# Kernel optimization log

Hardware: AMD Instinct MI355X
Metric: run time of the kernel (lower is better)

## Reference

```python
import jax, jax.numpy as jnp
import numpy as np

NUM_CLASSES = 10000
EMBED_DIM = 128
BATCH = 4096
SCALE = 10.0
FOCAL_ALPHA = 0.25
FOCAL_GAMMA = 2.0
HARD_NEG_RATIO = 0.3


def setup_inputs() -> dict:
    key = jax.random.key(0)
    k1, k2, k3, k4 = jax.random.split(key, 4)
    embeddings = jax.random.normal(k1, (BATCH, EMBED_DIM), dtype=jnp.float32)
    labels = jax.random.randint(k2, (BATCH,), 0, NUM_CLASSES)
    class_weights = jax.random.uniform(k3, (NUM_CLASSES,), dtype=jnp.float32)
    # kaiming_normal_(mode='fan_out') on [C, D] -> std = sqrt(2 / C)
    proxies = jax.random.normal(k4, (NUM_CLASSES, EMBED_DIM), dtype=jnp.float32) * np.sqrt(2.0 / NUM_CLASSES)
    return {"embeddings": embeddings, "labels": labels,
            "class_weights": class_weights, "proxies": proxies}


def reference(embeddings, labels, class_weights, proxies):
    C = proxies.shape[0]
    # L2 normalize (F.normalize with eps=1e-12)
    e = embeddings / jnp.maximum(jnp.linalg.norm(embeddings, axis=1, keepdims=True), 1e-12)
    p = proxies / jnp.maximum(jnp.linalg.norm(proxies, axis=1, keepdims=True), 1e-12)
    sim = jnp.einsum('bd,cd->bc', e, p) * SCALE  # [B, C]

    pos_sim = jnp.take_along_axis(sim, labels[:, None], axis=1)[:, 0]  # [B]

    # mask out the positive class, then top-k hard negatives (k is static)
    k = max(1, int((C - 1) * HARD_NEG_RATIO))
    is_pos = labels[:, None] == jnp.arange(C)[None, :]
    neg_sim = jnp.where(is_pos, -jnp.inf, sim)
    hard_neg, _ = jax.lax.top_k(neg_sim, k)  # [B, k]

    combined = jnp.concatenate([pos_sim[:, None], hard_neg], axis=1)  # [B, 1+k]
    probs = jax.nn.softmax(combined, axis=1)
    pos_prob = probs[:, 0]

    ce = -jnp.log(pos_prob + 1e-8)
    focal = FOCAL_ALPHA * (1.0 - pos_prob) ** FOCAL_GAMMA * ce
    weighted = focal * class_weights[labels]
    return jnp.sum(weighted) / embeddings.shape[0]
```

## Files before the change

### kernel.cpp

```cpp
#include <hip/hip_runtime.h>
#include <hip/hip_bf16.h>
#include <hip/hip_fp16.h>


#define BATCH   4096
#define NCLASS  10000
#define EDIM    128
#define KSEL    2999
#define LDK     136
#define MLOG    10.0f

typedef __attribute__((ext_vector_type(8))) short short8;
typedef __attribute__((ext_vector_type(4))) float floatx4;

__device__ __forceinline__ unsigned short f2bf(float f) {
    unsigned int u = __float_as_uint(f);
    unsigned int r = (u + 0x7FFFu + ((u >> 16) & 1u)) >> 16;
    return (unsigned short)r;
}
__device__ __forceinline__ unsigned int f2key16(float x) {
    unsigned short hb = __half_as_ushort(__float2half(x));
    return (hb & 0x8000u) ? (unsigned int)(~hb & 0xFFFFu)
                          : (unsigned int)(hb | 0x8000u);
}
__device__ __forceinline__ float key16val(unsigned int k) {
    unsigned short hb = (k & 0x8000u) ? (unsigned short)(k ^ 0x8000u)
                                      : (unsigned short)(~k & 0xFFFFu);
    return __half2float(__ushort_as_half(hb));
}

__global__ __launch_bounds__(256) void prep_kernel(
    const float* __restrict__ emb, const float* __restrict__ px,
    unsigned short* __restrict__ px_bf, unsigned short* __restrict__ emb_bf)
{
    const int tid  = threadIdx.x;
    const int lane = tid & 63;
    const int w    = tid >> 6;
    const int row  = blockIdx.x * 4 + w;

    const float* src;
    unsigned short* dst;
    float scale;
    if (row < NCLASS) {
        src = px + (size_t)row * EDIM;  dst = px_bf + (size_t)row * EDIM;  scale = 1.0f;
    } else {
        int r = row - NCLASS;
        src = emb + (size_t)r * EDIM;   dst = emb_bf + (size_t)r * EDIM;   scale = 10.0f;
    }
    float2 v = *(const float2*)(src + 2 * lane);
    float ss = v.x * v.x + v.y * v.y;
    #pragma unroll
    for (int off = 32; off; off >>= 1) ss += __shfl_xor(ss, off);
    float inv = scale / fmaxf(sqrtf(ss), 1e-12f);
    ushort2 o;
    o.x = f2bf(v.x * inv);
    o.y = f2bf(v.y * inv);
    *(ushort2*)(dst + 2 * lane) = o;
}

__global__ __launch_bounds__(256, 3) void gemm_kernel(
    const unsigned short* __restrict__ emb_bf,
    const unsigned short* __restrict__ px_bf,
    unsigned short* __restrict__ simk, int row0, int nby)
{
    __shared__ __align__(16) unsigned short T[128 * LDK];

    const int NBX = (NCLASS + 127) / 128;
    const int tid  = threadIdx.x;
    const int lane = tid & 63;
    const int w    = tid >> 6;

    int ct, rt;
    {
        int L = blockIdx.x;
        if ((nby & 7) == 0) {
            int rpx = nby >> 3;
            int xcd = L & 7;
            int s   = L >> 3;
            rt = xcd * rpx + (s % rpx);
            ct = s / rpx;
        } else {
            ct = L % NBX; rt = L / NBX;
        }
    }
    const int c0   = ct * 128;
    const int rg0  = row0 + rt * 128;

    const int wr = (w >> 1) * 64;
    const int wc = (w & 1) * 64;
    const int fm = lane & 15;
    const int fq = lane >> 4;

    const unsigned short* arow[4];
    const unsigned short* brow[4];
    #pragma unroll
    for (int i = 0; i < 4; ++i)
        arow[i] = emb_bf + (size_t)(rg0 + wr + i * 16 + fm) * EDIM + fq * 8;
    #pragma unroll
    for (int j = 0; j < 4; ++j) {
        int col = c0 + wc + j * 16 + fm;
        if (col > NCLASS - 1) col = NCLASS - 1;
        brow[j] = px_bf + (size_t)col * EDIM + fq * 8;
    }

    floatx4 acc[4][4];
    #pragma unroll
    for (int i = 0; i < 4; ++i)
        #pragma unroll
        for (int j = 0; j < 4; ++j)
            acc[i][j] = (floatx4){0.f, 0.f, 0.f, 0.f};

    short8 af[2][4], bf_[2][4];
    #pragma unroll
    for (int i = 0; i < 4; ++i) af[0][i]  = *(const short8*)(arow[i]);
    #pragma unroll
    for (int j = 0; j < 4; ++j) bf_[0][j] = *(const short8*)(brow[j]);

    #pragma unroll
    for (int kk = 0; kk < 4; ++kk) {
        const int cur = kk & 1, nxt = cur ^ 1;
        if (kk < 3) {
            const int kof = (kk + 1) * 32;
            #pragma unroll
            for (int i = 0; i < 4; ++i)
                af[nxt][i]  = *(const short8*)(arow[i] + kof);
            #pragma unroll
            for (int j = 0; j < 4; ++j)
                bf_[nxt][j] = *(const short8*)(brow[j] + kof);
        }
        #pragma unroll
        for (int i = 0; i < 4; ++i)
            #pragma unroll
            for (int j = 0; j < 4; ++j)
                acc[i][j] = __builtin_amdgcn_mfma_f32_16x16x32_bf16(
                    af[cur][i], bf_[cur][j], acc[i][j], 0, 0, 0);
    }

    #pragma unroll
    for (int j = 0; j < 4; ++j) {
        int col = wc + j * 16 + fm;
        #pragma unroll
        for (int i = 0; i < 4; ++i) {
            int rbase = wr + i * 16 + fq * 4;
            #pragma unroll
            for (int r = 0; r < 4; ++r)
                T[(rbase + r) * LDK + col] = (unsigned short)f2key16(acc[i][j][r]);
        }
    }
    __syncthreads();

    const int rl0 = rt * 128;
    #pragma unroll
    for (int t = 0; t < 8; ++t) {
        int idx = t * 256 + tid;
        int rowl = idx >> 4;
        int g    = idx & 15;
        int col  = c0 + g * 8;
        if (col < NCLASS) {
            uint4 v = *(const uint4*)(T + rowl * LDK + g * 8);
            *(uint4*)(simk + (size_t)(rl0 + rowl) * NCLASS + col) = v;
        }
    }
}

__global__ __launch_bounds__(256, 8) void select_kernel(
    const unsigned short* __restrict__ simk, const int* __restrict__ labels,
    const float* __restrict__ cw, float* __restrict__ partials, int row0)
{
    __shared__ __align__(16) unsigned int hist[2048];
    __shared__ __align__(16) unsigned int psum[256];
    __shared__ float fred[8];
    __shared__ float s_pos;
    __shared__ unsigned int s_b, s_fill, s_cntb;

    const int tid   = threadIdx.x;
    const int lane  = tid & 63;
    const int w     = tid >> 6;
    const int rl    = blockIdx.x;
    const int label = labels[row0 + rl];
    const unsigned short* srow = simk + (size_t)rl * NCLASS;

    unsigned short poskey = 0;
    if (tid == 0) poskey = srow[label];

    {
        uint4 z = make_uint4(0u, 0u, 0u, 0u);
        *(uint4*)&hist[tid * 8]     = z;
        *(uint4*)&hist[tid * 8 + 4] = z;
    }
    __syncthreads();
    uint4 kv[5];
    kv[4] = make_uint4(0u, 0u, 0u, 0u);
    #pragma unroll
    for (int t = 0; t < 5; ++t) {
        int i = tid + t * 256;
        if (i < NCLASS / 8) kv[t] = *(const uint4*)(srow + i * 8);
    }

    #pragma unroll
    for (int t = 0; t < 5; ++t) {
        int i = tid + t * 256;
        if (i < NCLASS / 8) {
            unsigned int p[4] = {kv[t].x, kv[t].y, kv[t].z, kv[t].w};
            #pragma unroll
            for (int q = 0; q < 4; ++q) {
                unsigned int klo = p[q] & 0xFFFFu;
                unsigned int khi = p[q] >> 16;
                atomicAdd(&hist[klo >> 5], 0x100000u | (klo & 31u));
                atomicAdd(&hist[khi >> 5], 0x100000u | (khi & 31u));
            }
        }
    }
    __syncthreads();
    if (tid == 0) {
        s_pos = key16val(poskey);
        hist[poskey >> 5] -= 0x100000u | ((unsigned int)poskey & 31u);
    }
    __syncthreads();

    uint4 h0 = *(const uint4*)&hist[tid * 8];
    uint4 h1 = *(const uint4*)&hist[tid * 8 + 4];
    unsigned int wd[8] = {h0.x, h0.y, h0.z, h0.w, h1.x, h1.y, h1.z, h1.w};
    unsigned int sfx[8];
    sfx[7] = wd[7] >> 20;
    #pragma unroll
    for (int i = 6; i >= 0; --i) sfx[i] = sfx[i + 1] + (wd[i] >> 20);
    psum[tid] = sfx[0];
    __syncthreads();
    if (w == 0) {
        uint4 g = *(const uint4*)&psum[lane * 4];
        unsigned int gs = g.x + g.y + g.z + g.w;
        unsigned int s = gs;
        #pragma unroll
        for (int off = 1; off < 64; off <<= 1) {
            unsigned int o = __shfl_down(s, off);
            if (lane + off < 64) s += o;
        }
        unsigned int above = s - gs;
        unsigned int a3 = above;
        unsigned int a2 = a3 + g.w;
        unsigned int a1 = a2 + g.z;
        unsigned int a0 = a1 + g.y;
        psum[lane * 4 + 0] = a0; psum[lane * 4 + 1] = a1;
        psum[lane * 4 + 2] = a2; psum[lane * 4 + 3] = a3;
    }
    __syncthreads();
    {
        unsigned int add = psum[tid];
        #pragma unroll
        for (int i = 0; i < 8; ++i) {
            unsigned int cur = sfx[i] + add;
            unsigned int nxt = ((i < 7) ? sfx[i + 1] : 0u) + add;
            if (cur >= KSEL && nxt < KSEL) {
                s_b    = (unsigned int)(tid * 8 + i);
                s_fill = KSEL - nxt;
                s_cntb = sfx[i] - ((i < 7) ? sfx[i + 1] : 0u);
            }
        }
    }
    __syncthreads();

    const unsigned int b = s_b;
    float sum = 0.f, bsum = 0.f;
    if (b >= 1024u) {
        const float fillf = (float)s_fill;
        #pragma unroll
        for (int i = 0; i < 8; ++i) {
            unsigned int bin = (unsigned int)(tid * 8 + i);
            unsigned int c = wd[i] >> 20;
            if (bin >= b && c) {
                float rbar = (float)(wd[i] & 0xFFFFFu) / (float)c;
                unsigned int kb = bin << 5;
                float v0  = key16val(kb);
                float v32 = key16val(kb + 32u);
                float vm  = v0 + (v32 - v0) * (rbar * 0.03125f);
                float e = __expf(vm - MLOG);
                sum += ((bin > b) ? (float)c : fillf) * e;
            }
        }
    } else {
        for (int i = tid; i < NCLASS / 8; i += 256) {
            uint4 pk = *(const uint4*)(srow + i * 8);
            unsigned int p[4] = {pk.x, pk.y, pk.z, pk.w};
            #pragma unroll
            for (int q = 0; q < 4; ++q) {
                unsigned int klo = p[q] & 0xFFFFu;
                unsigned int khi = p[q] >> 16;
                unsigned int blo = klo >> 5, bhi = khi >> 5;
                int idx = i * 8 + q * 2;
                if (blo >= b && idx != label) {
                    float e = __expf(key16val(klo) - MLOG);
                    if (blo > b) sum += e; else bsum += e;
                }
                if (bhi >= b && (idx + 1) != label) {
                    float e = __expf(key16val(khi) - MLOG);
                    if (bhi > b) sum += e; else bsum += e;
                }
            }
        }
    }
    #pragma unroll
    for (int off = 32; off; off >>= 1) {
        sum  += __shfl_xor(sum, off);
        bsum += __shfl_xor(bsum, off);
    }
    if (lane == 0) { fred[w] = sum; fred[4 + w] = bsum; }
    __syncthreads();

    if (tid == 0) {
        float S  = fred[0] + fred[1] + fred[2] + fred[3];
        float Bs = fred[4] + fred[5] + fred[6] + fred[7];
        float ep = __expf(s_pos - MLOG);
        float denom = S + Bs * ((float)s_fill / (float)s_cntb) + ep;
        float p  = ep / denom;
        float ce = -logf(p + 1e-8f);
        float focal = 0.25f * (1.0f - p) * (1.0f - p) * ce;
        partials[row0 + rl] = focal * cw[label] * (1.0f / (float)BATCH);
    }
}

__global__ __launch_bounds__(256) void reduce_kernel(
    const float* __restrict__ partials, float* __restrict__ out)
{
    __shared__ float red[4];
    const int tid = threadIdx.x;
    float s = 0.f;
    #pragma unroll
    for (int t = 0; t < BATCH / 256; ++t)
        s += partials[tid + t * 256];
    #pragma unroll
    for (int off = 32; off; off >>= 1) s += __shfl_xor(s, off);
    if ((tid & 63) == 0) red[tid >> 6] = s;
    __syncthreads();
    if (tid == 0) out[0] = red[0] + red[1] + red[2] + red[3];
}

extern "C" void kernel_launch(void* const* d_in, const int* in_sizes, int n_in,
                              void* d_out, int out_size, void* d_ws, size_t ws_size,
                              hipStream_t stream) {
    const float* emb    = (const float*)d_in[0];
    const int*   labels = (const int*)d_in[1];
    const float* cw     = (const float*)d_in[2];
    const float* px     = (const float*)d_in[3];
    float* out = (float*)d_out;
    char*  wsc = (char*)d_ws;

    unsigned short* px_bf  = (unsigned short*)wsc;
    unsigned short* emb_bf = (unsigned short*)(wsc + 2560000);
    float*          parts  = (float*)(wsc + 3608576);
    unsigned short* simk   = (unsigned short*)(wsc + 3624960);

    size_t fixed = 3624960;
    size_t avail = (ws_size > fixed) ? (ws_size - fixed) : 0;
    long long cap = (long long)(avail / ((size_t)NCLASS * 2));
    int chunk = (int)((cap / 128) * 128);
    if (chunk > BATCH) chunk = BATCH;
    if (chunk < 128) chunk = 128;

    prep_kernel<<<3524, 256, 0, stream>>>(emb, px, px_bf, emb_bf);

    const int NBX = (NCLASS + 127) / 128;
    for (int r0 = 0; r0 < BATCH; r0 += chunk) {
        int rows = (BATCH - r0 < chunk) ? (BATCH - r0) : chunk;
        int nby  = rows / 128;
        gemm_kernel<<<NBX * nby, 256, 0, stream>>>(emb_bf, px_bf, simk, r0, nby);
        select_kernel<<<rows, 256, 0, stream>>>(simk, labels, cw, parts, r0);
    }
    reduce_kernel<<<1, 256, 0, stream>>>(parts, out);
}
```

Baseline: 131.1 us.

## Stage proxy tile in LDS for GEMM and use nontemporal output stores

The GEMM kernel now loads the 128x128 bf16 proxy tile cooperatively into shared memory once. The MFMA loop reads B fragments from LDS instead of each wave fetching overlapping rows from global memory, and the same LDS buffer is reused for the output transpose after a barrier. It also raises the occupancy hint from 3 to 4 blocks per CU and writes the sim keys with nontemporal stores to reduce cache pollution. The cost is extra barriers and LDS traffic, and B is no longer prefetched ahead of use.

```diff
diff --git a/kernel.cpp b/kernel.cpp
--- a/kernel.cpp
+++ b/kernel.cpp
@@ -12,6 +12,7 @@
 
 typedef __attribute__((ext_vector_type(8))) short short8;
 typedef __attribute__((ext_vector_type(4))) float floatx4;
+typedef __attribute__((ext_vector_type(4))) unsigned int uintx4;
 
 __device__ __forceinline__ unsigned short f2bf(float f) {
     unsigned int u = __float_as_uint(f);
@@ -58,12 +59,12 @@
     *(ushort2*)(dst + 2 * lane) = o;
 }
 
-__global__ __launch_bounds__(256, 3) void gemm_kernel(
+__global__ __launch_bounds__(256, 4) void gemm_kernel(
     const unsigned short* __restrict__ emb_bf,
     const unsigned short* __restrict__ px_bf,
     unsigned short* __restrict__ simk, int row0, int nby)
 {
-    __shared__ __align__(16) unsigned short T[128 * LDK];
+    __shared__ __align__(16) unsigned short Bls[128 * LDK];
 
     const int NBX = (NCLASS + 127) / 128;
     const int tid  = threadIdx.x;
@@ -86,22 +87,32 @@
     const int c0   = ct * 128;
     const int rg0  = row0 + rt * 128;
 
+    #pragma unroll
+    for (int i = 0; i < 8; ++i) {
+        int c  = tid + i * 256;
+        int n  = c >> 4;
+        int kc = (c & 15) << 3;
+        uint4 v = make_uint4(0u, 0u, 0u, 0u);
+        if (c0 + n < NCLASS)
+            v = *(const uint4*)(px_bf + (size_t)(c0 + n) * EDIM + kc);
+        *(uint4*)(Bls + n * LDK + kc) = v;
+    }
+
     const int wr = (w >> 1) * 64;
     const int wc = (w & 1) * 64;
     const int fm = lane & 15;
     const int fq = lane >> 4;
 
     const unsigned short* arow[4];
-    const unsigned short* brow[4];
     #pragma unroll
     for (int i = 0; i < 4; ++i)
         arow[i] = emb_bf + (size_t)(rg0 + wr + i * 16 + fm) * EDIM + fq * 8;
-    #pragma unroll
-    for (int j = 0; j < 4; ++j) {
-        int col = c0 + wc + j * 16 + fm;
-        if (col > NCLASS - 1) col = NCLASS - 1;
-        brow[j] = px_bf + (size_t)col * EDIM + fq * 8;
-    }
+
+    short8 af[2][4];
+    #pragma unroll
+    for (int i = 0; i < 4; ++i) af[0][i] = *(const short8*)(arow[i]);
+
+    __syncthreads();
 
     floatx4 acc[4][4];
     #pragma unroll
@@ -109,33 +120,31 @@
         #pragma unroll
         for (int j = 0; j < 4; ++j)
             acc[i][j] = (floatx4){0.f, 0.f, 0.f, 0.f};
-
-    short8 af[2][4], bf_[2][4];
-    #pragma unroll
-    for (int i = 0; i < 4; ++i) af[0][i]  = *(const short8*)(arow[i]);
-    #pragma unroll
-    for (int j = 0; j < 4; ++j) bf_[0][j] = *(const short8*)(brow[j]);
 
     #pragma unroll
     for (int kk = 0; kk < 4; ++kk) {
         const int cur = kk & 1, nxt = cur ^ 1;
         if (kk < 3) {
-            const int kof = (kk + 1) * 32;
+            const int kof2 = (kk + 1) * 32;
             #pragma unroll
             for (int i = 0; i < 4; ++i)
-                af[nxt][i]  = *(const short8*)(arow[i] + kof);
-            #pragma unroll
-            for (int j = 0; j < 4; ++j)
-                bf_[nxt][j] = *(const short8*)(brow[j] + kof);
-        }
+                af[nxt][i] = *(const short8*)(arow[i] + kof2);
+        }
+        const int kof = kk * 32 + fq * 8;
+        short8 b[4];
+        #pragma unroll
+        for (int j = 0; j < 4; ++j)
+            b[j] = *(const short8*)(Bls + (wc + j * 16 + fm) * LDK + kof);
         #pragma unroll
         for (int i = 0; i < 4; ++i)
             #pragma unroll
             for (int j = 0; j < 4; ++j)
                 acc[i][j] = __builtin_amdgcn_mfma_f32_16x16x32_bf16(
-                    af[cur][i], bf_[cur][j], acc[i][j], 0, 0, 0);
-    }
-
+                    af[cur][i], b[j], acc[i][j], 0, 0, 0);
+    }
+
+    __syncthreads();
+    unsigned short* T = Bls;
     #pragma unroll
     for (int j = 0; j < 4; ++j) {
         int col = wc + j * 16 + fm;
@@ -157,8 +166,9 @@
         int g    = idx & 15;
         int col  = c0 + g * 8;
         if (col < NCLASS) {
-            uint4 v = *(const uint4*)(T + rowl * LDK + g * 8);
-            *(uint4*)(simk + (size_t)(rl0 + rowl) * NCLASS + col) = v;
+            uintx4 v = *(const uintx4*)(T + rowl * LDK + g * 8);
+            __builtin_nontemporal_store(v,
+                (uintx4*)(simk + (size_t)(rl0 + rowl) * NCLASS + col));
         }
     }
 }
```

New measurement: 139.5 us. 1.06x slower.

## Stage GEMM tiles into LDS via direct global-to-LDS loads with XOR swizzle

Applied to the files above, without the earlier changes.

The GEMM kernel now copies the full 128x128 A and B bf16 tiles into shared memory with global_load_lds (16-byte direct loads) using an XOR swizzle, then reads MFMA fragments from LDS instead of loading them from global memory into registers per wave. The goal is to remove duplicated global loads across waves and the register double-buffering, and to make the tile fetch coalesced. The output staging buffer now reuses the A tile region without padding, which may cause bank conflicts on the transpose writes. Shared memory grows to 64KB, and the occupancy hint of 3 blocks is dropped, which may lower occupancy.

```diff
diff --git a/kernel.cpp b/kernel.cpp
--- a/kernel.cpp
+++ b/kernel.cpp
@@ -7,7 +7,6 @@
 #define NCLASS  10000
 #define EDIM    128
 #define KSEL    2999
-#define LDK     136
 #define MLOG    10.0f
 
 typedef __attribute__((ext_vector_type(8))) short short8;
@@ -27,6 +26,13 @@
     unsigned short hb = (k & 0x8000u) ? (unsigned short)(k ^ 0x8000u)
                                       : (unsigned short)(~k & 0xFFFFu);
     return __half2float(__ushort_as_half(hb));
+}
+
+__device__ __forceinline__ void gload16(const unsigned short* g,
+                                        unsigned short* l) {
+    __builtin_amdgcn_global_load_lds(
+        (const __attribute__((address_space(1))) unsigned int*)g,
+        (__attribute__((address_space(3))) unsigned int*)l, 16, 0, 0);
 }
 
 __global__ __launch_bounds__(256) void prep_kernel(
@@ -58,12 +64,13 @@
     *(ushort2*)(dst + 2 * lane) = o;
 }
 
-__global__ __launch_bounds__(256, 3) void gemm_kernel(
+__global__ __launch_bounds__(256) void gemm_kernel(
     const unsigned short* __restrict__ emb_bf,
     const unsigned short* __restrict__ px_bf,
     unsigned short* __restrict__ simk, int row0, int nby)
 {
-    __shared__ __align__(16) unsigned short T[128 * LDK];
+    __shared__ __align__(16) unsigned short Als[128 * EDIM];
+    __shared__ __align__(16) unsigned short Bls[128 * EDIM];
 
     const int NBX = (NCLASS + 127) / 128;
     const int tid  = threadIdx.x;
@@ -86,23 +93,29 @@
     const int c0   = ct * 128;
     const int rg0  = row0 + rt * 128;
 
+    #pragma unroll
+    for (int i = 0; i < 8; ++i) {
+        int c   = tid + i * 256;
+        int r   = c >> 4;
+        int gsw = (c & 15) ^ (r & 7);
+        gload16(emb_bf + (size_t)(rg0 + r) * EDIM + gsw * 8, Als + c * 8);
+    }
+    #pragma unroll
+    for (int i = 0; i < 8; ++i) {
+        int c   = tid + i * 256;
+        int n   = c >> 4;
+        int gsw = (c & 15) ^ (n & 7);
+        int col = c0 + n;
+        if (col > NCLASS - 1) col = NCLASS - 1;
+        gload16(px_bf + (size_t)col * EDIM + gsw * 8, Bls + c * 8);
+    }
+    __syncthreads();
+
     const int wr = (w >> 1) * 64;
     const int wc = (w & 1) * 64;
     const int fm = lane & 15;
     const int fq = lane >> 4;
 
-    const unsigned short* arow[4];
-    const unsigned short* brow[4];
-    #pragma unroll
-    for (int i = 0; i < 4; ++i)
-        arow[i] = emb_bf + (size_t)(rg0 + wr + i * 16 + fm) * EDIM + fq * 8;
-    #pragma unroll
-    for (int j = 0; j < 4; ++j) {
-        int col = c0 + wc + j * 16 + fm;
-        if (col > NCLASS - 1) col = NCLASS - 1;
-        brow[j] = px_bf + (size_t)col * EDIM + fq * 8;
-    }
-
     floatx4 acc[4][4];
     #pragma unroll
     for (int i = 0; i < 4; ++i)
@@ -110,32 +123,26 @@
         for (int j = 0; j < 4; ++j)
             acc[i][j] = (floatx4){0.f, 0.f, 0.f, 0.f};
 
-    short8 af[2][4], bf_[2][4];
-    #pragma unroll
-    for (int i = 0; i < 4; ++i) af[0][i]  = *(const short8*)(arow[i]);
-    #pragma unroll
-    for (int j = 0; j < 4; ++j) bf_[0][j] = *(const short8*)(brow[j]);
-
     #pragma unroll
     for (int kk = 0; kk < 4; ++kk) {
-        const int cur = kk & 1, nxt = cur ^ 1;
-        if (kk < 3) {
-            const int kof = (kk + 1) * 32;
-            #pragma unroll
-            for (int i = 0; i < 4; ++i)
-                af[nxt][i]  = *(const short8*)(arow[i] + kof);
-            #pragma unroll
-            for (int j = 0; j < 4; ++j)
-                bf_[nxt][j] = *(const short8*)(brow[j] + kof);
-        }
+        const int go = ((kk * 4 + fq) ^ (fm & 7)) << 3;
+        short8 a[4], b[4];
+        #pragma unroll
+        for (int i = 0; i < 4; ++i)
+            a[i] = *(const short8*)(Als + (wr + i * 16 + fm) * EDIM + go);
+        #pragma unroll
+        for (int j = 0; j < 4; ++j)
+            b[j] = *(const short8*)(Bls + (wc + j * 16 + fm) * EDIM + go);
         #pragma unroll
         for (int i = 0; i < 4; ++i)
             #pragma unroll
             for (int j = 0; j < 4; ++j)
                 acc[i][j] = __builtin_amdgcn_mfma_f32_16x16x32_bf16(
-                    af[cur][i], bf_[cur][j], acc[i][j], 0, 0, 0);
-    }
-
+                    a[i], b[j], acc[i][j], 0, 0, 0);
+    }
+
+    __syncthreads();
+    unsigned short* T = Als;
     #pragma unroll
     for (int j = 0; j < 4; ++j) {
         int col = wc + j * 16 + fm;
@@ -144,7 +151,7 @@
             int rbase = wr + i * 16 + fq * 4;
             #pragma unroll
             for (int r = 0; r < 4; ++r)
-                T[(rbase + r) * LDK + col] = (unsigned short)f2key16(acc[i][j][r]);
+                T[(rbase + r) * 128 + col] = (unsigned short)f2key16(acc[i][j][r]);
         }
     }
     __syncthreads();
@@ -157,7 +164,7 @@
         int g    = idx & 15;
         int col  = c0 + g * 8;
         if (col < NCLASS) {
-            uint4 v = *(const uint4*)(T + rowl * LDK + g * 8);
+            uint4 v = *(const uint4*)(T + rowl * 128 + g * 8);
             *(uint4*)(simk + (size_t)(rl0 + rowl) * NCLASS + col) = v;
         }
     }
```

Result: faster. 115.4 us (-12.0%).
